# Kernel optimization log

Measured on AMD Instinct MI355X. Metric: run time of the kernel, lower is better.

Reference implementation:

```python
import jax, jax.numpy as jnp
import numpy as np

D_MODEL = 4096
NUM_EXPERTS = 64


def setup_inputs() -> dict:
    key = jax.random.key(0)
    kx, kw, kb = jax.random.split(key, 3)
    x = jax.random.normal(kx, (4, 4096, D_MODEL), dtype=jnp.float32)
    # nn.Linear(d_model, num_experts): weight [E, D], bias [E]
    bound = 1.0 / np.sqrt(D_MODEL)
    W = jax.random.uniform(kw, (NUM_EXPERTS, D_MODEL), dtype=jnp.float32, minval=-bound, maxval=bound)
    b = jax.random.uniform(kb, (NUM_EXPERTS,), dtype=jnp.float32, minval=-bound, maxval=bound)
    return {"x": x, "W": W, "b": b}


def reference(x, W, b):
    # logits: [B, S, E]
    logits = jnp.einsum('bsd,ed->bse', x, W) + b
    scores = jax.nn.softmax(logits, axis=-1)
    val, idx = jax.lax.top_k(scores, 2)            # [B, S, 2]
    # scatter top-2 values back into a dense [B, S, E] dispatch mask
    onehot = jax.nn.one_hot(idx, NUM_EXPERTS, dtype=scores.dtype)  # [B, S, 2, E]
    dispatch = jnp.einsum('bsk,bske->bse', val, onehot)
    combine = dispatch
    expert_counts = dispatch.sum(axis=(0, 1))      # [E]
    return dispatch, combine, expert_counts
```

## Files before the change

### kernel.cpp

```cpp
#include <hip/hip_runtime.h>
#include <math.h>

#define D_MODEL 4096
#define NEXP    64
#define NTOK    16384
#define NSL     4
#define NCH     4
#define KS      256
#define BMT     256

typedef __attribute__((ext_vector_type(8))) short  bf16x8;
typedef __attribute__((ext_vector_type(4))) float  f32x4;

__device__ __forceinline__ unsigned short f2bf_rn(float f) {
    union { float f; unsigned u; } v; v.f = f;
    unsigned r = v.u + 0x7fffu + ((v.u >> 16) & 1u);
    return (unsigned short)(r >> 16);
}
__device__ __forceinline__ float bf2f(unsigned short h) {
    union { unsigned u; float f; } v; v.u = ((unsigned)h) << 16;
    return v.f;
}
__device__ __forceinline__ void split2(float f0, float f1, unsigned& hw, unsigned& lw) {
    unsigned short h0 = f2bf_rn(f0), h1 = f2bf_rn(f1);
    unsigned short l0 = f2bf_rn(f0 - bf2f(h0)), l1 = f2bf_rn(f1 - bf2f(h1));
    hw = (unsigned)h0 | ((unsigned)h1 << 16);
    lw = (unsigned)l0 | ((unsigned)l1 << 16);
}

__global__ __launch_bounds__(256)
void k0_prep(const float* __restrict__ W, unsigned short* __restrict__ ws,
             float* __restrict__ logits, float* __restrict__ out) {
    const int gid = blockIdx.x * 256 + threadIdx.x;
    if (blockIdx.x == 0 && threadIdx.x < NEXP)
        out[(size_t)2 * NTOK * NEXP + threadIdx.x] = 0.f;
    float4 z = make_float4(0.f, 0.f, 0.f, 0.f);
    float* lz = logits + (size_t)gid * 16;
#pragma unroll
    for (int k = 0; k < 4; ++k)
        *reinterpret_cast<float4*>(&lz[k * 4]) = z;
    int i = gid * 4;
    float4 v = *reinterpret_cast<const float4*>(&W[i]);
    unsigned short h[4], l[4];
    float f[4] = {v.x, v.y, v.z, v.w};
#pragma unroll
    for (int k = 0; k < 4; ++k) {
        h[k] = f2bf_rn(f[k]);
        l[k] = f2bf_rn(f[k] - bf2f(h[k]));
    }
    *reinterpret_cast<short4*>(&ws[i])                  = make_short4(h[0], h[1], h[2], h[3]);
    *reinterpret_cast<short4*>(&ws[NEXP * D_MODEL + i]) = make_short4(l[0], l[1], l[2], l[3]);
}

__global__ __launch_bounds__(512, 4)
void k1_gemm(const float* __restrict__ x, const unsigned short* __restrict__ wsplit,
             float* __restrict__ logits) {
    __shared__ uint4 whi[NEXP * 32];
    __shared__ uint4 wlo[NEXP * 32];

    const int tid = threadIdx.x;
    const int t0  = (blockIdx.x >> 2) * BMT;
    const int sp  = blockIdx.x & 3;

    const int lane = tid & 63;
    const int rowl = lane & 15;
    const int grp  = lane >> 4;
    const int wtok = t0 + (tid >> 6) * 32;

    f32x4 acc[2][4];
#pragma unroll
    for (int m = 0; m < 2; ++m)
#pragma unroll
        for (int n = 0; n < 4; ++n)
            acc[m][n] = (f32x4){0.f, 0.f, 0.f, 0.f};

    for (int half = 0; half < NCH; ++half) {
        const int ks0 = (sp * NCH + half) * KS;
        if (half) __syncthreads();

#pragma unroll
        for (int i = 0; i < 4; ++i) {
            int p  = tid + i * 512;
            int e  = p >> 5;
            int c  = p & 31;
            int cs = (c & 24) | ((c & 7) ^ (e & 7));
            const unsigned short* src = wsplit + (size_t)e * D_MODEL + ks0 + c * 8;
            whi[e * 32 + cs] = *reinterpret_cast<const uint4*>(src);
            wlo[e * 32 + cs] = *reinterpret_cast<const uint4*>(src + NEXP * D_MODEL);
        }
        __syncthreads();

        const float* xp0 = x + (size_t)(wtok + rowl) * D_MODEL + ks0 + grp * 8;
        const float* xp1 = xp0 + (size_t)16 * D_MODEL;

#pragma unroll
        for (int kb = 0; kb < 8; ++kb) {
            union { bf16x8 v; unsigned u[4]; } ah0, al0, ah1, al1;
            {
                f32x4 c0 = *reinterpret_cast<const f32x4*>(xp0 + kb * 32);
                f32x4 c1 = *reinterpret_cast<const f32x4*>(xp0 + kb * 32 + 4);
                split2(c0.x, c0.y, ah0.u[0], al0.u[0]);
                split2(c0.z, c0.w, ah0.u[1], al0.u[1]);
                split2(c1.x, c1.y, ah0.u[2], al0.u[2]);
                split2(c1.z, c1.w, ah0.u[3], al0.u[3]);
            }
            {
                f32x4 c0 = *reinterpret_cast<const f32x4*>(xp1 + kb * 32);
                f32x4 c1 = *reinterpret_cast<const f32x4*>(xp1 + kb * 32 + 4);
                split2(c0.x, c0.y, ah1.u[0], al1.u[0]);
                split2(c0.z, c0.w, ah1.u[1], al1.u[1]);
                split2(c1.x, c1.y, ah1.u[2], al1.u[2]);
                split2(c1.z, c1.w, ah1.u[3], al1.u[3]);
            }
            const int c  = kb * 4 + grp;
            const int cs = (c & 24) | ((c & 7) ^ (rowl & 7));
#pragma unroll
            for (int n = 0; n < 4; ++n) {
                const int idx = (n * 16 + rowl) * 32 + cs;
                bf16x8 bh = *reinterpret_cast<const bf16x8*>(&whi[idx]);
                bf16x8 bl = *reinterpret_cast<const bf16x8*>(&wlo[idx]);
                acc[0][n] = __builtin_amdgcn_mfma_f32_16x16x32_bf16(ah0.v, bh, acc[0][n], 0, 0, 0);
                acc[0][n] = __builtin_amdgcn_mfma_f32_16x16x32_bf16(ah0.v, bl, acc[0][n], 0, 0, 0);
                acc[0][n] = __builtin_amdgcn_mfma_f32_16x16x32_bf16(al0.v, bh, acc[0][n], 0, 0, 0);
                acc[1][n] = __builtin_amdgcn_mfma_f32_16x16x32_bf16(ah1.v, bh, acc[1][n], 0, 0, 0);
                acc[1][n] = __builtin_amdgcn_mfma_f32_16x16x32_bf16(ah1.v, bl, acc[1][n], 0, 0, 0);
                acc[1][n] = __builtin_amdgcn_mfma_f32_16x16x32_bf16(al1.v, bh, acc[1][n], 0, 0, 0);
            }
        }
    }

#pragma unroll
    for (int m = 0; m < 2; ++m)
#pragma unroll
        for (int n = 0; n < 4; ++n)
#pragma unroll
            for (int i = 0; i < 4; ++i) {
                const int t = wtok + m * 16 + grp * 4 + i;
                const int e = n * 16 + rowl;
                atomicAdd(&logits[(size_t)t * NEXP + e], acc[m][n][i]);
            }
}

__global__ __launch_bounds__(128)
void k2_softmax_top2(const float* __restrict__ logits, const float* __restrict__ bias,
                     float* __restrict__ out) {
    const int t = blockIdx.x * 128 + threadIdx.x;
    __shared__ float cnt[NEXP];
    __shared__ float bs[NEXP];
    if (threadIdx.x < NEXP) {
        cnt[threadIdx.x] = 0.f;
        bs[threadIdx.x]  = bias[threadIdx.x];
    }
    __syncthreads();

    float l[NEXP];
    const float* lp = logits + (size_t)t * NEXP;
#pragma unroll
    for (int g = 0; g < 16; ++g) {
        float4 v = *reinterpret_cast<const float4*>(&lp[g * 4]);
        l[4 * g + 0] = v.x + bs[4 * g + 0];
        l[4 * g + 1] = v.y + bs[4 * g + 1];
        l[4 * g + 2] = v.z + bs[4 * g + 2];
        l[4 * g + 3] = v.w + bs[4 * g + 3];
    }

    float m = l[0];
#pragma unroll
    for (int e = 1; e < NEXP; ++e) m = fmaxf(m, l[e]);

    float sum = 0.f;
#pragma unroll
    for (int e = 0; e < NEXP; ++e) sum += __expf(l[e] - m);

    float v1 = -INFINITY, v2 = -INFINITY;
    int   i1 = 0, i2 = 0;
#pragma unroll
    for (int e = 0; e < NEXP; ++e) {
        if (l[e] > v1) { v2 = v1; i2 = i1; v1 = l[e]; i1 = e; }
        else if (l[e] > v2) { v2 = l[e]; i2 = e; }
    }
    const float inv = 1.f / sum;
    const float s1 = __expf(v1 - m) * inv;
    const float s2 = __expf(v2 - m) * inv;

    float* disp = out + (size_t)t * NEXP;
    float* comb = out + (size_t)NTOK * NEXP + (size_t)t * NEXP;
#pragma unroll
    for (int g = 0; g < 16; ++g) {
        float4 o = make_float4(0.f, 0.f, 0.f, 0.f);
        if ((i1 >> 2) == g) (&o.x)[i1 & 3] = s1;
        if ((i2 >> 2) == g) (&o.x)[i2 & 3] = s2;
        *reinterpret_cast<float4*>(&disp[g * 4]) = o;
        *reinterpret_cast<float4*>(&comb[g * 4]) = o;
    }

    atomicAdd(&cnt[i1], s1);
    atomicAdd(&cnt[i2], s2);
    __syncthreads();
    if (threadIdx.x < NEXP)
        atomicAdd(&out[(size_t)2 * NTOK * NEXP + threadIdx.x], cnt[threadIdx.x]);
}

extern "C" void kernel_launch(void* const* d_in, const int* in_sizes, int n_in,
                              void* d_out, int out_size, void* d_ws, size_t ws_size,
                              hipStream_t stream) {
    const float* x = (const float*)d_in[0];
    const float* W = (const float*)d_in[1];
    const float* b = (const float*)d_in[2];
    float* out = (float*)d_out;
    unsigned short* ws = (unsigned short*)d_ws;
    float* logits = (float*)(ws + 2 * NEXP * D_MODEL);

    k0_prep<<<256, 256, 0, stream>>>(W, ws, logits, out);
    k1_gemm<<<(NTOK / BMT) * NSL, 512, 0, stream>>>(x, ws, logits);
    k2_softmax_top2<<<NTOK / 128, 128, 0, stream>>>(logits, b, out);
}
```

Baseline: 101.6 us.

## Software-pipeline x loads with inline asm double buffering and split K across eight slices

The GEMM's inner loop now issues raw global_load_dwordx4 instructions two k-steps ahead, using two register buffers and explicit vmcnt waits, so the fp32-to-bf16 split and the MFMAs overlap with memory latency. The K dimension is also split into 8 slices of 2 chunks instead of 4 of 4, which doubles the grid size but also doubles the atomic adds into the logits. The inline asm bypasses compiler scheduling, so correctness depends on the vmcnt counts matching the number of outstanding loads.

```diff
diff --git a/kernel.cpp b/kernel.cpp
--- a/kernel.cpp
+++ b/kernel.cpp
@@ -4,8 +4,8 @@
 #define D_MODEL 4096
 #define NEXP    64
 #define NTOK    16384
-#define NSL     4
-#define NCH     4
+#define NSL     8
+#define NCH     2
 #define KS      256
 #define BMT     256
 
@@ -27,6 +27,12 @@
     hw = (unsigned)h0 | ((unsigned)h1 << 16);
     lw = (unsigned)l0 | ((unsigned)l1 << 16);
 }
+__device__ __forceinline__ void gload16(f32x4& r, const float* p) {
+    asm volatile("global_load_dwordx4 %0, %1, off" : "=v"(r) : "v"(p));
+}
+
+#define WAITV_(n) asm volatile("s_waitcnt vmcnt(" #n ")" ::: "memory")
+#define WAITV(n)  WAITV_(n)
 
 __global__ __launch_bounds__(256)
 void k0_prep(const float* __restrict__ W, unsigned short* __restrict__ ws,
@@ -59,8 +65,8 @@
     __shared__ uint4 wlo[NEXP * 32];
 
     const int tid = threadIdx.x;
-    const int t0  = (blockIdx.x >> 2) * BMT;
-    const int sp  = blockIdx.x & 3;
+    const int t0  = (blockIdx.x >> 3) * BMT;
+    const int sp  = blockIdx.x & 7;
 
     const int lane = tid & 63;
     const int rowl = lane & 15;
@@ -73,6 +79,40 @@
 #pragma unroll
         for (int n = 0; n < 4; ++n)
             acc[m][n] = (f32x4){0.f, 0.f, 0.f, 0.f};
+
+#define STEPX(kb, WN, c0, c1, c2, c3, DOI) do {                              \
+    WAITV(WN);                                                               \
+    __builtin_amdgcn_sched_barrier(0);                                       \
+    union { bf16x8 v; unsigned u[4]; } ah0, al0, ah1, al1;                   \
+    split2(c0.x, c0.y, ah0.u[0], al0.u[0]);                                  \
+    split2(c0.z, c0.w, ah0.u[1], al0.u[1]);                                  \
+    split2(c1.x, c1.y, ah0.u[2], al0.u[2]);                                  \
+    split2(c1.z, c1.w, ah0.u[3], al0.u[3]);                                  \
+    split2(c2.x, c2.y, ah1.u[0], al1.u[0]);                                  \
+    split2(c2.z, c2.w, ah1.u[1], al1.u[1]);                                  \
+    split2(c3.x, c3.y, ah1.u[2], al1.u[2]);                                  \
+    split2(c3.z, c3.w, ah1.u[3], al1.u[3]);                                  \
+    if (DOI) {                                                               \
+        gload16(c0, xp0 + ((kb) + 2) * 32);                                  \
+        gload16(c1, xp0 + ((kb) + 2) * 32 + 4);                              \
+        gload16(c2, xp1 + ((kb) + 2) * 32);                                  \
+        gload16(c3, xp1 + ((kb) + 2) * 32 + 4);                              \
+    }                                                                        \
+    const int c  = (kb) * 4 + grp;                                           \
+    const int cs = (c & 24) | ((c & 7) ^ (rowl & 7));     \
+    _Pragma("unroll")                                                        \
+    for (int n = 0; n < 4; ++n) {                                            \
+        const int idx = (n * 16 + rowl) * 32 + cs;                           \
+        bf16x8 bh = *reinterpret_cast<const bf16x8*>(&whi[idx]);             \
+        bf16x8 bl = *reinterpret_cast<const bf16x8*>(&wlo[idx]);             \
+        acc[0][n] = __builtin_amdgcn_mfma_f32_16x16x32_bf16(ah0.v, bh, acc[0][n], 0, 0, 0); \
+        acc[0][n] = __builtin_amdgcn_mfma_f32_16x16x32_bf16(ah0.v, bl, acc[0][n], 0, 0, 0); \
+        acc[0][n] = __builtin_amdgcn_mfma_f32_16x16x32_bf16(al0.v, bh, acc[0][n], 0, 0, 0); \
+        acc[1][n] = __builtin_amdgcn_mfma_f32_16x16x32_bf16(ah1.v, bh, acc[1][n], 0, 0, 0); \
+        acc[1][n] = __builtin_amdgcn_mfma_f32_16x16x32_bf16(ah1.v, bl, acc[1][n], 0, 0, 0); \
+        acc[1][n] = __builtin_amdgcn_mfma_f32_16x16x32_bf16(al1.v, bh, acc[1][n], 0, 0, 0); \
+    }                                                                        \
+} while (0)
 
     for (int half = 0; half < NCH; ++half) {
         const int ks0 = (sp * NCH + half) * KS;
@@ -93,40 +133,20 @@
         const float* xp0 = x + (size_t)(wtok + rowl) * D_MODEL + ks0 + grp * 8;
         const float* xp1 = xp0 + (size_t)16 * D_MODEL;
 
-#pragma unroll
-        for (int kb = 0; kb < 8; ++kb) {
-            union { bf16x8 v; unsigned u[4]; } ah0, al0, ah1, al1;
-            {
-                f32x4 c0 = *reinterpret_cast<const f32x4*>(xp0 + kb * 32);
-                f32x4 c1 = *reinterpret_cast<const f32x4*>(xp0 + kb * 32 + 4);
-                split2(c0.x, c0.y, ah0.u[0], al0.u[0]);
-                split2(c0.z, c0.w, ah0.u[1], al0.u[1]);
-                split2(c1.x, c1.y, ah0.u[2], al0.u[2]);
-                split2(c1.z, c1.w, ah0.u[3], al0.u[3]);
-            }
-            {
-                f32x4 c0 = *reinterpret_cast<const f32x4*>(xp1 + kb * 32);
-                f32x4 c1 = *reinterpret_cast<const f32x4*>(xp1 + kb * 32 + 4);
-                split2(c0.x, c0.y, ah1.u[0], al1.u[0]);
-                split2(c0.z, c0.w, ah1.u[1], al1.u[1]);
-                split2(c1.x, c1.y, ah1.u[2], al1.u[2]);
-                split2(c1.z, c1.w, ah1.u[3], al1.u[3]);
-            }
-            const int c  = kb * 4 + grp;
-            const int cs = (c & 24) | ((c & 7) ^ (rowl & 7));
-#pragma unroll
-            for (int n = 0; n < 4; ++n) {
-                const int idx = (n * 16 + rowl) * 32 + cs;
-                bf16x8 bh = *reinterpret_cast<const bf16x8*>(&whi[idx]);
-                bf16x8 bl = *reinterpret_cast<const bf16x8*>(&wlo[idx]);
-                acc[0][n] = __builtin_amdgcn_mfma_f32_16x16x32_bf16(ah0.v, bh, acc[0][n], 0, 0, 0);
-                acc[0][n] = __builtin_amdgcn_mfma_f32_16x16x32_bf16(ah0.v, bl, acc[0][n], 0, 0, 0);
-                acc[0][n] = __builtin_amdgcn_mfma_f32_16x16x32_bf16(al0.v, bh, acc[0][n], 0, 0, 0);
-                acc[1][n] = __builtin_amdgcn_mfma_f32_16x16x32_bf16(ah1.v, bh, acc[1][n], 0, 0, 0);
-                acc[1][n] = __builtin_amdgcn_mfma_f32_16x16x32_bf16(ah1.v, bl, acc[1][n], 0, 0, 0);
-                acc[1][n] = __builtin_amdgcn_mfma_f32_16x16x32_bf16(al1.v, bh, acc[1][n], 0, 0, 0);
-            }
-        }
+        f32x4 xA0, xA1, xA2, xA3, xB0, xB1, xB2, xB3;
+        gload16(xA0, xp0);      gload16(xA1, xp0 + 4);
+        gload16(xA2, xp1);      gload16(xA3, xp1 + 4);
+        gload16(xB0, xp0 + 32); gload16(xB1, xp0 + 36);
+        gload16(xB2, xp1 + 32); gload16(xB3, xp1 + 36);
+
+        STEPX(0, 4, xA0, xA1, xA2, xA3, 1);
+        STEPX(1, 4, xB0, xB1, xB2, xB3, 1);
+        STEPX(2, 4, xA0, xA1, xA2, xA3, 1);
+        STEPX(3, 4, xB0, xB1, xB2, xB3, 1);
+        STEPX(4, 4, xA0, xA1, xA2, xA3, 1);
+        STEPX(5, 4, xB0, xB1, xB2, xB3, 1);
+        STEPX(6, 4, xA0, xA1, xA2, xA3, 0);
+        STEPX(7, 0, xB0, xB1, xB2, xB3, 0);
     }
 
 #pragma unroll
```

Measured after the change: 86.78 us. -14.6%, faster.
